# Optimization experiments

Hardware: AMD Instinct MI355X
Metric: run time of the kernel (lower is better)

Reference implementation:

```python
import math
import jax, jax.numpy as jnp
import numpy as np

N = 50000
C = 128      # in_channels == out_channels
H = 8        # nhead
D = C // H   # head_dim = 16
E = 800000


def _layernorm(x, g, b, eps=1e-5):
    mu = jnp.mean(x, axis=-1, keepdims=True)
    var = jnp.var(x, axis=-1, keepdims=True)
    return (x - mu) * jax.lax.rsqrt(var + eps) * g + b


def setup_inputs() -> dict:
    key = jax.random.key(0)
    ks = jax.random.split(key, 12)
    s = 1.0 / math.sqrt(C)          # ~xavier scale
    s4 = 1.0 / math.sqrt(4 * C)
    return {
        "x": jax.random.normal(ks[0], (N, C), dtype=jnp.float32),
        "edge_index": jax.random.randint(ks[1], (2, E), 0, N, dtype=jnp.int64),
        "Wq": jax.random.normal(ks[2], (C, C), dtype=jnp.float32) * s,
        "Wk": jax.random.normal(ks[3], (C, C), dtype=jnp.float32) * s,
        "Wv": jax.random.normal(ks[4], (C, C), dtype=jnp.float32) * s,
        "Wo": jax.random.normal(ks[5], (C, C), dtype=jnp.float32) * s,
        "bo": jnp.zeros((C,), dtype=jnp.float32),
        "Wf1": jax.random.normal(ks[6], (C, 4 * C), dtype=jnp.float32) * s,
        "bf1": jnp.zeros((4 * C,), dtype=jnp.float32),
        "Wf2": jax.random.normal(ks[7], (4 * C, C), dtype=jnp.float32) * s4,
        "bf2": jnp.zeros((C,), dtype=jnp.float32),
        "g1": jnp.ones((C,), dtype=jnp.float32),
        "b1": jnp.zeros((C,), dtype=jnp.float32),
        "g2": jnp.ones((C,), dtype=jnp.float32),
        "b2": jnp.zeros((C,), dtype=jnp.float32),
    }


def reference(x, edge_index, Wq, Wk, Wv, Wo, bo, Wf1, bf1, Wf2, bf2, g1, b1, g2, b2):
    n = x.shape[0]
    loops = jnp.arange(n, dtype=edge_index.dtype)
    row = jnp.concatenate([edge_index[0], loops])  # source nodes
    col = jnp.concatenate([edge_index[1], loops])  # destination nodes

    q = (x @ Wq).reshape(n, H, D)
    k = (x @ Wk).reshape(n, H, D)
    v = (x @ Wv).reshape(n, H, D)

    # edge-level attention scores [E+N, H]
    scores = jnp.einsum('ehd,ehd->eh', q[row], k[col]) / math.sqrt(D)
    smax = jax.ops.segment_max(scores, col, num_segments=n)  # every node has a self-loop
    exp = jnp.exp(scores - smax[col])
    ssum = jax.ops.segment_sum(exp, col, num_segments=n)
    alpha = exp / (ssum[col] + 1e-8)

    out = jax.ops.segment_sum(v[row] * alpha[..., None], col, num_segments=n)
    attn = out.reshape(n, C) @ Wo + bo

    residual = x  # input_proj is Identity (in_channels == out_channels)
    x1 = _layernorm(residual + attn, g1, b1)
    ffn = jax.nn.gelu(x1 @ Wf1 + bf1, approximate=False) @ Wf2 + bf2
    return _layernorm(x1 + ffn, g2, b2)
```

## Files before the change

kernel.cpp:

```cpp
#include <hip/hip_runtime.h>
#include <cmath>


typedef short bf16x8 __attribute__((ext_vector_type(8)));
typedef float f32x4 __attribute__((ext_vector_type(4)));
typedef unsigned int uint_as1 __attribute__((address_space(1)));
typedef unsigned int uint_as3 __attribute__((address_space(3)));

__device__ inline unsigned short f2bf(float f) {
    unsigned int u = __float_as_uint(f);
    u += 0x7fffu + ((u >> 16) & 1u);
    return (unsigned short)(u >> 16);
}
__device__ inline float bflo(unsigned int w) { return __uint_as_float(w << 16); }
__device__ inline float bfhi(unsigned int w) { return __uint_as_float(w & 0xffff0000u); }

__device__ inline void gload16(const unsigned short* g, unsigned short* l) {
    __builtin_amdgcn_global_load_lds((const uint_as1*)g, (uint_as3*)l, 16, 0, 0);
}

__device__ inline float gelu_f(float x) {
    float ax = fabsf(x) * 0.70710678118f;
    float t = __builtin_amdgcn_rcpf(fmaf(0.3275911f, ax, 1.0f));
    float p = fmaf(1.061405429f, t, -1.453152027f);
    p = fmaf(p, t, 1.421413741f);
    p = fmaf(p, t, -0.284496736f);
    p = fmaf(p, t, 0.254829592f);
    p = p * t;
    float e = __expf(-ax * ax);
    float pe = p * e;
    float w = (x >= 0.f) ? (2.0f - pe) : pe;
    return 0.5f * x * w;
}


__device__ __forceinline__ void stage_panel(unsigned short* Bs,
                                            const unsigned short* base,
                                            int strideK) {
    int tid = threadIdx.x;
    int srow = tid >> 4, cc = tid & 15;
    int gc = (cc & ~7) | ((cc & 7) ^ (srow & 7));
    const unsigned short* src = base + (size_t)srow * strideK + gc * 8;
    unsigned short* dst = Bs + srow * 128 + cc * 8;
#pragma unroll
    for (int j = 0; j < 8; ++j)
        gload16(src + (size_t)j * 16 * strideK, dst + j * 16 * 128);
}

__device__ __forceinline__ void loadA_g(bf16x8 (&af)[4][4],
                                        const unsigned short* A, int M,
                                        int m0, int wr, int l16, int quad) {
#pragma unroll
    for (int ti = 0; ti < 4; ++ti) {
        int row = m0 + wr * 64 + ti * 16 + l16;
        if (row > M - 1) row = M - 1;
        const unsigned short* ar = A + (size_t)row * 128 + quad * 8;
#pragma unroll
        for (int j = 0; j < 4; ++j) af[ti][j] = *(const bf16x8*)(ar + j * 32);
    }
}

__device__ __forceinline__ void mm16(f32x4 (&acc)[4][4], const bf16x8 (&af)[4][4],
                                     const unsigned short* Bs,
                                     int wc, int quad, int l16) {
#pragma unroll
    for (int ks = 0; ks < 4; ++ks) {
        bf16x8 bfr[4];
#pragma unroll
        for (int tj = 0; tj < 4; ++tj) {
            int nr = wc * 64 + tj * 16 + l16;
            int cidx = ks * 4 + quad;
            int slot = (cidx & ~7) | ((cidx & 7) ^ (nr & 7));
            bfr[tj] = *(const bf16x8*)&Bs[nr * 128 + slot * 8];
        }
#pragma unroll
        for (int ti = 0; ti < 4; ++ti)
#pragma unroll
            for (int tj = 0; tj < 4; ++tj)
                acc[ti][tj] = __builtin_amdgcn_mfma_f32_16x16x32_bf16(
                    af[ti][ks], bfr[tj], acc[ti][tj], 0, 0, 0);
    }
}


__global__ __launch_bounds__(256) void k_init(
    const float* __restrict__ x, unsigned short* __restrict__ xb,
    const float* __restrict__ Wq, const float* __restrict__ Wk,
    const float* __restrict__ Wv, const float* __restrict__ Wo,
    const float* __restrict__ Wf1, const float* __restrict__ Wf2,
    unsigned short* __restrict__ Wqkvt, unsigned short* __restrict__ Wot,
    unsigned short* __restrict__ Wf1t, unsigned short* __restrict__ Wf2t,
    int* __restrict__ cursor, int4* __restrict__ csrz,
    int N, int nCsr4, int nCast) {
    int bid = blockIdx.x;
    int t = threadIdx.x;

    int NBc = (N + 255) >> 8;
    if (bid < NBc) {
        int i = bid * 256 + t;
        if (i < N) cursor[i] = 0;
        return;
    }
    bid -= NBc;
    int NBz = (nCsr4 + 255) >> 8;
    if (bid < NBz) {
        int i = bid * 256 + t;
        if (i < nCsr4) csrz[i] = make_int4(0, 0, 0, 0);
        return;
    }
    bid -= NBz;
    if (bid < nCast) {
        int i = bid * 256 + t;
        if (i < N * 32) {
            float4 v = ((const float4*)x)[i];
            ushort4 o;
            o.x = f2bf(v.x); o.y = f2bf(v.y); o.z = f2bf(v.z); o.w = f2bf(v.w);
            ((ushort4*)xb)[i] = o;
        }
        return;
    }
    bid -= nCast;
    int z, idx;
    if (bid < 256) { z = bid >> 6; idx = (bid & 63) * 256 + t; }
    else           { z = 4 + ((bid - 256) >> 8); idx = ((bid - 256) & 255) * 256 + t; }

    const float* in; unsigned short* out; int K, Co;
    switch (z) {
        case 0: in = Wq;  out = Wqkvt; K = 128; Co = 128; break;
        case 1: in = Wk;  out = Wqkvt; K = 128; Co = 128; break;
        case 2: in = Wv;  out = Wqkvt; K = 128; Co = 128; break;
        case 3: in = Wo;  out = Wot;   K = 128; Co = 128; break;
        case 4: in = Wf1; out = Wf1t;  K = 128; Co = 512; break;
        default: in = Wf2; out = Wf2t; K = 512; Co = 128; break;
    }
    if (idx >= K * Co) return;
    int k = idx / Co, c = idx % Co;
    int row;
    switch (z) {
        case 0: row = ((c >> 1) << 2) | (c & 1); break;
        case 1: row = 256 + c; break;
        case 2: row = (((c >> 1) << 2) | (c & 1)) + 2; break;
        default: row = c; break;
    }
    out[(size_t)row * K + k] = f2bf(in[idx]);
}


__global__ __launch_bounds__(256) void k_fq(
    const int* __restrict__ ei, int* __restrict__ cursor,
    unsigned short* __restrict__ csr, int E, int N,
    const unsigned short* __restrict__ xb, const unsigned short* __restrict__ Wqkvt,
    unsigned short* __restrict__ qkv, int nFillB, int Mt) {
    __shared__ unsigned short smem[128 * 136];

    if ((int)blockIdx.x < nFillB) {
        int e = blockIdx.x * 256 + threadIdx.x;
        if (e < E + N) {
            int row, col;
            if (e < E) { row = ei[e]; col = ei[E + e]; }
            else       { row = col = e - E; }
            int pos = atomicAdd(&cursor[col], 1);
            csr[(size_t)col * 64 + pos] = (unsigned short)row;
        }
        return;
    }

    int bid = blockIdx.x - nFillB;
    int z = bid / Mt, mt = bid % Mt;
    int m0 = mt * 128, n0 = z * 128;

    int tid = threadIdx.x;
    int wid = tid >> 6, lane = tid & 63;
    int quad = lane >> 4, l16 = lane & 15;
    int wr = wid >> 1, wc = wid & 1;

    bf16x8 af[4][4];
    loadA_g(af, xb, N, m0, wr, l16, quad);
    stage_panel(smem, Wqkvt + (size_t)n0 * 128, 128);
    __syncthreads();

    f32x4 acc[4][4];
#pragma unroll
    for (int i = 0; i < 4; ++i)
#pragma unroll
        for (int j = 0; j < 4; ++j) acc[i][j] = {0.f, 0.f, 0.f, 0.f};
    mm16(acc, af, smem, wc, quad, l16);

    __syncthreads();
#pragma unroll
    for (int ti = 0; ti < 4; ++ti)
#pragma unroll
        for (int tj = 0; tj < 4; ++tj) {
            int c = wc * 64 + tj * 16 + l16;
#pragma unroll
            for (int r = 0; r < 4; ++r) {
                int rl = wr * 64 + ti * 16 + quad * 4 + r;
                smem[rl * 136 + c] = f2bf(acc[ti][tj][r]);
            }
        }
    __syncthreads();
    int rl = tid >> 1, half = tid & 1;
    int grow = m0 + rl;
    if (grow < N) {
#pragma unroll
        for (int c8 = 0; c8 < 8; ++c8) {
            uint4 v = *(const uint4*)&smem[rl * 136 + half * 64 + c8 * 8];
            *(uint4*)&qkv[(size_t)grow * 384 + n0 + half * 64 + c8 * 8] = v;
        }
    }
}


__global__ __launch_bounds__(256) void k_attn(
    const unsigned int* __restrict__ qkv, const int* __restrict__ counts,
    const unsigned short* __restrict__ csr, unsigned int* __restrict__ ob,
    int N) {
    int j = blockIdx.x * 4 + (threadIdx.x >> 6);
    if (j >= N) return;
    int l = threadIdx.x & 63;
    int lk = l & 31;
    int half = l >> 5;
    const uint4* qv4 = (const uint4*)qkv;

    uint2 kw = *(const uint2*)(qkv + (size_t)j * 192 + 128 + lk * 2);
    const float S = 0.36067376022224085f;
    float k0 = bflo(kw.x) * S, k1 = bfhi(kw.x) * S;
    float k2 = bflo(kw.y) * S, k3 = bfhi(kw.y) * S;

    int cnt = counts[j];
    int nb = (cnt + 3) >> 2;
    const unsigned short* cp = csr + (size_t)j * 64;

    int ra0 = cp[half],     rb0 = cp[2 + half];
    int ra1 = cp[4 + half], rb1 = cp[6 + half];
    uint4 gA = qv4[(unsigned)ra0 * 48u + lk];
    uint4 gB = qv4[(unsigned)rb0 * 48u + lk];

    float lsum = 0.f, a0 = 0.f, a1 = 0.f, a2 = 0.f, a3 = 0.f;
    for (int bi = 0; bi < nb; ++bi) {
        int ra2 = cp[(bi + 2) * 4 + half];
        int rb2 = cp[(bi + 2) * 4 + 2 + half];
        uint4 nA = qv4[(unsigned)ra1 * 48u + lk];
        uint4 nB = qv4[(unsigned)rb1 * 48u + lk];

        int rem = cnt - bi * 4;
        {
            float s = fmaf(bflo(gA.x), k0,
                      fmaf(bfhi(gA.x), k1,
                      fmaf(bflo(gA.z), k2, bfhi(gA.z) * k3)));
            s += __shfl_xor(s, 1);
            s += __shfl_xor(s, 2);
            float e = exp2f(s);
            e = (half < rem) ? e : 0.f;
            lsum += e;
            a0 = fmaf(e, bflo(gA.y), a0); a1 = fmaf(e, bfhi(gA.y), a1);
            a2 = fmaf(e, bflo(gA.w), a2); a3 = fmaf(e, bfhi(gA.w), a3);
        }
        {
            float s = fmaf(bflo(gB.x), k0,
                      fmaf(bfhi(gB.x), k1,
                      fmaf(bflo(gB.z), k2, bfhi(gB.z) * k3)));
            s += __shfl_xor(s, 1);
            s += __shfl_xor(s, 2);
            float e = exp2f(s);
            e = (2 + half < rem) ? e : 0.f;
            lsum += e;
            a0 = fmaf(e, bflo(gB.y), a0); a1 = fmaf(e, bfhi(gB.y), a1);
            a2 = fmaf(e, bflo(gB.w), a2); a3 = fmaf(e, bfhi(gB.w), a3);
        }
        gA = nA; gB = nB; ra1 = ra2; rb1 = rb2;
    }

    lsum += __shfl_xor(lsum, 32);
    a0 += __shfl_xor(a0, 32); a1 += __shfl_xor(a1, 32);
    a2 += __shfl_xor(a2, 32); a3 += __shfl_xor(a3, 32);

    if (half == 0) {
        float inv = 1.f / (lsum + 1e-8f);
        uint2 o;
        o.x = ((unsigned int)f2bf(a1 * inv) << 16) | (unsigned int)f2bf(a0 * inv);
        o.y = ((unsigned int)f2bf(a3 * inv) << 16) | (unsigned int)f2bf(a2 * inv);
        *(uint2*)(ob + (size_t)j * 64 + lk * 2) = o;
    }
}


__global__ __launch_bounds__(256) void k_tail(
    const unsigned short* __restrict__ ob, const unsigned short* __restrict__ Wot,
    const float* __restrict__ bo, const float* __restrict__ x,
    const float* __restrict__ g1, const float* __restrict__ b1,
    const unsigned short* __restrict__ Wf1t, const float* __restrict__ bf1,
    const unsigned short* __restrict__ Wf2t, const float* __restrict__ bf2,
    const float* __restrict__ g2, const float* __restrict__ b2,
    float* __restrict__ dout, int M) {
    __shared__ unsigned short Bs[128 * 128];
    __shared__ unsigned short Ls[128 * 136];
    __shared__ float X1[128 * 132];
    __shared__ float pS[2][128], pQ[2][128];

    int tid = threadIdx.x;
    int wid = tid >> 6, lane = tid & 63;
    int quad = lane >> 4, l16 = lane & 15;
    int wr = wid >> 1, wc = wid & 1;
    int m0 = blockIdx.x * 128;

    float gv1[4], bv1[4], gv2[4], bv2[4], bi[4];
#pragma unroll
    for (int tj = 0; tj < 4; ++tj) {
        int col = wc * 64 + tj * 16 + l16;
        gv1[tj] = g1[col]; bv1[tj] = b1[col];
        gv2[tj] = g2[col]; bv2[tj] = b2[col];
        bi[tj] = bo[col];
    }

    {
        bf16x8 af[4][4];
        loadA_g(af, ob, M, m0, wr, l16, quad);
        stage_panel(Bs, Wot, 128);
        __syncthreads();

        f32x4 acc[4][4];
#pragma unroll
        for (int i = 0; i < 4; ++i)
#pragma unroll
            for (int j = 0; j < 4; ++j) acc[i][j] = {0.f, 0.f, 0.f, 0.f};
        mm16(acc, af, Bs, wc, quad, l16);

#pragma unroll
        for (int ti = 0; ti < 4; ++ti)
#pragma unroll
            for (int tj = 0; tj < 4; ++tj) {
                int col = wc * 64 + tj * 16 + l16;
#pragma unroll
                for (int r = 0; r < 4; ++r) {
                    int row = m0 + wr * 64 + ti * 16 + quad * 4 + r;
                    float rv = (row < M) ? x[(size_t)row * 128 + col] : 0.f;
                    acc[ti][tj][r] += bi[tj] + rv;
                }
            }
#pragma unroll
        for (int ti = 0; ti < 4; ++ti)
#pragma unroll
            for (int r = 0; r < 4; ++r) {
                float s = acc[ti][0][r] + acc[ti][1][r] + acc[ti][2][r] + acc[ti][3][r];
                float q = acc[ti][0][r] * acc[ti][0][r] + acc[ti][1][r] * acc[ti][1][r]
                        + acc[ti][2][r] * acc[ti][2][r] + acc[ti][3][r] * acc[ti][3][r];
                s += __shfl_xor(s, 1); q += __shfl_xor(q, 1);
                s += __shfl_xor(s, 2); q += __shfl_xor(q, 2);
                s += __shfl_xor(s, 4); q += __shfl_xor(q, 4);
                s += __shfl_xor(s, 8); q += __shfl_xor(q, 8);
                if (l16 == 0) {
                    int lr = wr * 64 + ti * 16 + quad * 4 + r;
                    pS[wc][lr] = s; pQ[wc][lr] = q;
                }
            }
        __syncthreads();
        if (tid < 128) {
            float s = pS[0][tid] + pS[1][tid];
            float q = pQ[0][tid] + pQ[1][tid];
            float mean = s * 0.0078125f;
            float var = q * 0.0078125f - mean * mean;
            pS[0][tid] = mean;
            pQ[0][tid] = rsqrtf(var + 1e-5f);
        }
        __syncthreads();
#pragma unroll
        for (int ti = 0; ti < 4; ++ti)
#pragma unroll
            for (int r = 0; r < 4; ++r) {
                int lr = wr * 64 + ti * 16 + quad * 4 + r;
                float mean = pS[0][lr], rs = pQ[0][lr];
#pragma unroll
                for (int tj = 0; tj < 4; ++tj) {
                    int col = wc * 64 + tj * 16 + l16;
                    float y = (acc[ti][tj][r] - mean) * rs * gv1[tj] + bv1[tj];
                    X1[lr * 132 + col] = y;
                    Ls[lr * 136 + col] = f2bf(y);
                }
            }
    }
    __syncthreads();

    bf16x8 ax1[4][4];
#pragma unroll
    for (int ti = 0; ti < 4; ++ti) {
        int rl = wr * 64 + ti * 16 + l16;
#pragma unroll
        for (int j = 0; j < 4; ++j)
            ax1[ti][j] = *(const bf16x8*)&Ls[rl * 136 + j * 32 + quad * 8];
    }

    f32x4 dacc[4][4];
#pragma unroll
    for (int i = 0; i < 4; ++i)
#pragma unroll
        for (int j = 0; j < 4; ++j) dacc[i][j] = {0.f, 0.f, 0.f, 0.f};

    for (int c = 0; c < 4; ++c) {
        __syncthreads();
        stage_panel(Bs, Wf1t + (size_t)c * 128 * 128, 128);
        __syncthreads();

        f32x4 hacc[4][4];
#pragma unroll
        for (int i = 0; i < 4; ++i)
#pragma unroll
            for (int j = 0; j < 4; ++j) hacc[i][j] = {0.f, 0.f, 0.f, 0.f};
        mm16(hacc, ax1, Bs, wc, quad, l16);

#pragma unroll
        for (int ti = 0; ti < 4; ++ti)
#pragma unroll
            for (int tj = 0; tj < 4; ++tj) {
                float bb = bf1[c * 128 + wc * 64 + tj * 16 + l16];
#pragma unroll
                for (int r = 0; r < 4; ++r) {
                    int rl = wr * 64 + ti * 16 + quad * 4 + r;
                    Ls[rl * 136 + wc * 64 + tj * 16 + l16] =
                        f2bf(gelu_f(hacc[ti][tj][r] + bb));
                }
            }
        __syncthreads();

        bf16x8 ah[4][4];
#pragma unroll
        for (int ti = 0; ti < 4; ++ti) {
            int rl = wr * 64 + ti * 16 + l16;
#pragma unroll
            for (int j = 0; j < 4; ++j)
                ah[ti][j] = *(const bf16x8*)&Ls[rl * 136 + j * 32 + quad * 8];
        }
        __syncthreads();
        stage_panel(Bs, Wf2t + (size_t)c * 128, 512);
        __syncthreads();
        mm16(dacc, ah, Bs, wc, quad, l16);
    }

#pragma unroll
    for (int ti = 0; ti < 4; ++ti)
#pragma unroll
        for (int tj = 0; tj < 4; ++tj) {
            int col = wc * 64 + tj * 16 + l16;
            float bb = bf2[col];
#pragma unroll
            for (int r = 0; r < 4; ++r) {
                int lr = wr * 64 + ti * 16 + quad * 4 + r;
                dacc[ti][tj][r] += bb + X1[lr * 132 + col];
            }
        }
#pragma unroll
    for (int ti = 0; ti < 4; ++ti)
#pragma unroll
        for (int r = 0; r < 4; ++r) {
            float s = dacc[ti][0][r] + dacc[ti][1][r] + dacc[ti][2][r] + dacc[ti][3][r];
            float q = dacc[ti][0][r] * dacc[ti][0][r] + dacc[ti][1][r] * dacc[ti][1][r]
                    + dacc[ti][2][r] * dacc[ti][2][r] + dacc[ti][3][r] * dacc[ti][3][r];
            s += __shfl_xor(s, 1); q += __shfl_xor(q, 1);
            s += __shfl_xor(s, 2); q += __shfl_xor(q, 2);
            s += __shfl_xor(s, 4); q += __shfl_xor(q, 4);
            s += __shfl_xor(s, 8); q += __shfl_xor(q, 8);
            if (l16 == 0) {
                int lr = wr * 64 + ti * 16 + quad * 4 + r;
                pS[wc][lr] = s; pQ[wc][lr] = q;
            }
        }
    __syncthreads();
    if (tid < 128) {
        float s = pS[0][tid] + pS[1][tid];
        float q = pQ[0][tid] + pQ[1][tid];
        float mean = s * 0.0078125f;
        float var = q * 0.0078125f - mean * mean;
        pS[0][tid] = mean;
        pQ[0][tid] = rsqrtf(var + 1e-5f);
    }
    __syncthreads();
#pragma unroll
    for (int ti = 0; ti < 4; ++ti)
#pragma unroll
        for (int r = 0; r < 4; ++r) {
            int lr = wr * 64 + ti * 16 + quad * 4 + r;
            int row = m0 + lr;
            if (row >= M) continue;
            float mean = pS[0][lr], rs = pQ[0][lr];
#pragma unroll
            for (int tj = 0; tj < 4; ++tj) {
                int col = wc * 64 + tj * 16 + l16;
                dout[(size_t)row * 128 + col] =
                    (dacc[ti][tj][r] - mean) * rs * gv2[tj] + bv2[tj];
            }
        }
}


extern "C" void kernel_launch(void* const* d_in, const int* in_sizes, int n_in,
                              void* d_out, int out_size, void* d_ws, size_t ws_size,
                              hipStream_t stream) {
    const float* x   = (const float*)d_in[0];
    const int* ei    = (const int*)d_in[1];
    const float* Wq  = (const float*)d_in[2];
    const float* Wk  = (const float*)d_in[3];
    const float* Wv  = (const float*)d_in[4];
    const float* Wo  = (const float*)d_in[5];
    const float* bo  = (const float*)d_in[6];
    const float* Wf1 = (const float*)d_in[7];
    const float* bf1 = (const float*)d_in[8];
    const float* Wf2 = (const float*)d_in[9];
    const float* bf2 = (const float*)d_in[10];
    const float* g1  = (const float*)d_in[11];
    const float* b1  = (const float*)d_in[12];
    const float* g2  = (const float*)d_in[13];
    const float* b2  = (const float*)d_in[14];

    int N = in_sizes[0] / 128;
    int E = in_sizes[1] / 2;
    int N2 = ((N + 127) / 128) * 128;
    int NE = E + N;

    char* p = (char*)d_ws;
    auto alloc = [&](size_t bytes) -> char* {
        char* r = p;
        p += (bytes + 255) & ~(size_t)255;
        return r;
    };
    unsigned short* qkv = (unsigned short*)alloc((size_t)N2 * 384 * 2);
    unsigned short* ob  = (unsigned short*)alloc((size_t)N2 * 128 * 2);
    unsigned short* xb  = (unsigned short*)alloc((size_t)N2 * 128 * 2);
    unsigned short* Wqkvt = (unsigned short*)alloc(384 * 128 * 2);
    unsigned short* Wot   = (unsigned short*)alloc(128 * 128 * 2);
    unsigned short* Wf1t  = (unsigned short*)alloc(512 * 128 * 2);
    unsigned short* Wf2t  = (unsigned short*)alloc(128 * 512 * 2);
    int* cursor = (int*)alloc((size_t)N * 4);
    unsigned short* csr = (unsigned short*)alloc(((size_t)N * 64 + 256) * 2);

    int nCsr4 = N * 8 + 32;
    int nCast = (N * 32 + 255) / 256;
    int nInit = ((N + 255) / 256) + ((nCsr4 + 255) / 256) + nCast + 768;
    int M128 = (N + 127) / 128;
    int nFillB = (NE + 255) / 256;

    k_init<<<nInit, 256, 0, stream>>>(x, xb, Wq, Wk, Wv, Wo, Wf1, Wf2,
                                      Wqkvt, Wot, Wf1t, Wf2t,
                                      cursor, (int4*)csr, N, nCsr4, nCast);

    k_fq<<<nFillB + 3 * M128, 256, 0, stream>>>(ei, cursor, csr, E, N,
                                                xb, Wqkvt, qkv, nFillB, M128);

    k_attn<<<(N + 3) / 4, 256, 0, stream>>>((const unsigned int*)qkv, cursor,
                                            csr, (unsigned int*)ob, N);

    k_tail<<<M128, 256, 0, stream>>>(ob, Wot, bo, x, g1, b1,
                                     Wf1t, bf1, Wf2t, bf2, g2, b2,
                                     (float*)d_out, N);
}
```

Baseline: 349.2 us.

## Cut k_tail LDS footprint for two blocks per CU and interleave CSR fill with QKV GEMM

k_tail drops its padded Ls and fp32 X1 shared buffers. The LayerNorm-1 output is written to a new global fp32 buffer and read back for the second residual. The GELU hidden tile is kept in a swizzled LDS buffer and consumed by a new mm16_AL that loads A fragments straight from LDS. With the smaller LDS use and launch_bounds(256,2), two blocks can share a CU. Separately, k_fq interleaves edge-fill blocks with GEMM blocks (one GEMM per four block ids) so atomics and matmul overlap, at the cost of extra global traffic for x1 and some redundant empty blocks.

```diff
diff --git a/kernel.cpp b/kernel.cpp
--- a/kernel.cpp
+++ b/kernel.cpp
@@ -82,6 +82,36 @@
     }
 }
 
+__device__ __forceinline__ void mm16_AL(f32x4 (&acc)[4][4],
+                                        const unsigned short* Hs,
+                                        const unsigned short* Bs,
+                                        int wr, int wc, int quad, int l16) {
+#pragma unroll
+    for (int ks = 0; ks < 4; ++ks) {
+        int cidx = ks * 4 + quad;
+        bf16x8 afr[4];
+#pragma unroll
+        for (int ti = 0; ti < 4; ++ti) {
+            int rl = wr * 64 + ti * 16 + l16;
+            int slot = (cidx & ~7) | ((cidx & 7) ^ (rl & 7));
+            afr[ti] = *(const bf16x8*)&Hs[rl * 128 + slot * 8];
+        }
+        bf16x8 bfr[4];
+#pragma unroll
+        for (int tj = 0; tj < 4; ++tj) {
+            int nr = wc * 64 + tj * 16 + l16;
+            int slot = (cidx & ~7) | ((cidx & 7) ^ (nr & 7));
+            bfr[tj] = *(const bf16x8*)&Bs[nr * 128 + slot * 8];
+        }
+#pragma unroll
+        for (int ti = 0; ti < 4; ++ti)
+#pragma unroll
+            for (int tj = 0; tj < 4; ++tj)
+                acc[ti][tj] = __builtin_amdgcn_mfma_f32_16x16x32_bf16(
+                    afr[ti], bfr[tj], acc[ti][tj], 0, 0, 0);
+    }
+}
+
 
 __global__ __launch_bounds__(256) void k_init(
     const float* __restrict__ x, unsigned short* __restrict__ xb,
@@ -153,8 +183,11 @@
     unsigned short* __restrict__ qkv, int nFillB, int Mt) {
     __shared__ unsigned short smem[128 * 136];
 
-    if ((int)blockIdx.x < nFillB) {
-        int e = blockIdx.x * 256 + threadIdx.x;
+    int bid = blockIdx.x;
+    if (bid & 3) {
+        int fi = bid - (bid >> 2) - 1;
+        if (fi >= nFillB) return;
+        int e = fi * 256 + threadIdx.x;
         if (e < E + N) {
             int row, col;
             if (e < E) { row = ei[e]; col = ei[E + e]; }
@@ -165,8 +198,8 @@
         return;
     }
 
-    int bid = blockIdx.x - nFillB;
-    int z = bid / Mt, mt = bid % Mt;
+    int qb = bid >> 2;
+    int z = qb / Mt, mt = qb % Mt;
     int m0 = mt * 128, n0 = z * 128;
 
     int tid = threadIdx.x;
@@ -285,17 +318,17 @@
 }
 
 
-__global__ __launch_bounds__(256) void k_tail(
+__global__ __launch_bounds__(256, 2) void k_tail(
     const unsigned short* __restrict__ ob, const unsigned short* __restrict__ Wot,
     const float* __restrict__ bo, const float* __restrict__ x,
     const float* __restrict__ g1, const float* __restrict__ b1,
+    float* __restrict__ x1f,
     const unsigned short* __restrict__ Wf1t, const float* __restrict__ bf1,
     const unsigned short* __restrict__ Wf2t, const float* __restrict__ bf2,
     const float* __restrict__ g2, const float* __restrict__ b2,
     float* __restrict__ dout, int M) {
     __shared__ unsigned short Bs[128 * 128];
-    __shared__ unsigned short Ls[128 * 136];
-    __shared__ float X1[128 * 132];
+    __shared__ unsigned short Hs[128 * 128];
     __shared__ float pS[2][128], pQ[2][128];
 
     int tid = threadIdx.x;
@@ -304,15 +337,6 @@
     int wr = wid >> 1, wc = wid & 1;
     int m0 = blockIdx.x * 128;
 
-    float gv1[4], bv1[4], gv2[4], bv2[4], bi[4];
-#pragma unroll
-    for (int tj = 0; tj < 4; ++tj) {
-        int col = wc * 64 + tj * 16 + l16;
-        gv1[tj] = g1[col]; bv1[tj] = b1[col];
-        gv2[tj] = g2[col]; bv2[tj] = b2[col];
-        bi[tj] = bo[col];
-    }
-
     {
         bf16x8 af[4][4];
         loadA_g(af, ob, M, m0, wr, l16, quad);
@@ -331,11 +355,12 @@
 #pragma unroll
             for (int tj = 0; tj < 4; ++tj) {
                 int col = wc * 64 + tj * 16 + l16;
+                float bb = bo[col];
 #pragma unroll
                 for (int r = 0; r < 4; ++r) {
                     int row = m0 + wr * 64 + ti * 16 + quad * 4 + r;
                     float rv = (row < M) ? x[(size_t)row * 128 + col] : 0.f;
-                    acc[ti][tj][r] += bi[tj] + rv;
+                    acc[ti][tj][r] += bb + rv;
                 }
             }
 #pragma unroll
@@ -369,13 +394,16 @@
 #pragma unroll
             for (int r = 0; r < 4; ++r) {
                 int lr = wr * 64 + ti * 16 + quad * 4 + r;
+                int row = m0 + lr;
                 float mean = pS[0][lr], rs = pQ[0][lr];
 #pragma unroll
                 for (int tj = 0; tj < 4; ++tj) {
                     int col = wc * 64 + tj * 16 + l16;
-                    float y = (acc[ti][tj][r] - mean) * rs * gv1[tj] + bv1[tj];
-                    X1[lr * 132 + col] = y;
-                    Ls[lr * 136 + col] = f2bf(y);
+                    float y = (acc[ti][tj][r] - mean) * rs * g1[col] + b1[col];
+                    if (row < M) x1f[(size_t)row * 128 + col] = y;
+                    int ch = col >> 3;
+                    int sc = (ch & ~7) | ((ch & 7) ^ (lr & 7));
+                    Hs[lr * 128 + sc * 8 + (col & 7)] = f2bf(y);
                 }
             }
     }
@@ -386,8 +414,11 @@
     for (int ti = 0; ti < 4; ++ti) {
         int rl = wr * 64 + ti * 16 + l16;
 #pragma unroll
-        for (int j = 0; j < 4; ++j)
-            ax1[ti][j] = *(const bf16x8*)&Ls[rl * 136 + j * 32 + quad * 8];
+        for (int j = 0; j < 4; ++j) {
+            int cidx = j * 4 + quad;
+            int slot = (cidx & ~7) | ((cidx & 7) ^ (rl & 7));
+            ax1[ti][j] = *(const bf16x8*)&Hs[rl * 128 + slot * 8];
+        }
     }
 
     f32x4 dacc[4][4];
@@ -407,33 +438,27 @@
 #pragma unroll
             for (int j = 0; j < 4; ++j) hacc[i][j] = {0.f, 0.f, 0.f, 0.f};
         mm16(hacc, ax1, Bs, wc, quad, l16);
+        __syncthreads();
 
 #pragma unroll
         for (int ti = 0; ti < 4; ++ti)
 #pragma unroll
             for (int tj = 0; tj < 4; ++tj) {
-                float bb = bf1[c * 128 + wc * 64 + tj * 16 + l16];
+                int cc = wc * 64 + tj * 16 + l16;
+                float bb = bf1[c * 128 + cc];
 #pragma unroll
                 for (int r = 0; r < 4; ++r) {
                     int rl = wr * 64 + ti * 16 + quad * 4 + r;
-                    Ls[rl * 136 + wc * 64 + tj * 16 + l16] =
+                    int ch = cc >> 3;
+                    int sc = (ch & ~7) | ((ch & 7) ^ (rl & 7));
+                    Hs[rl * 128 + sc * 8 + (cc & 7)] =
                         f2bf(gelu_f(hacc[ti][tj][r] + bb));
                 }
             }
-        __syncthreads();
-
-        bf16x8 ah[4][4];
-#pragma unroll
-        for (int ti = 0; ti < 4; ++ti) {
-            int rl = wr * 64 + ti * 16 + l16;
-#pragma unroll
-            for (int j = 0; j < 4; ++j)
-                ah[ti][j] = *(const bf16x8*)&Ls[rl * 136 + j * 32 + quad * 8];
-        }
-        __syncthreads();
         stage_panel(Bs, Wf2t + (size_t)c * 128, 512);
         __syncthreads();
-        mm16(dacc, ah, Bs, wc, quad, l16);
+
+        mm16_AL(dacc, Hs, Bs, wr, wc, quad, l16);
     }
 
 #pragma unroll
@@ -444,8 +469,9 @@
             float bb = bf2[col];
 #pragma unroll
             for (int r = 0; r < 4; ++r) {
-                int lr = wr * 64 + ti * 16 + quad * 4 + r;
-                dacc[ti][tj][r] += bb + X1[lr * 132 + col];
+                int row = m0 + wr * 64 + ti * 16 + quad * 4 + r;
+                float rv = (row < M) ? x1f[(size_t)row * 128 + col] : 0.f;
+                dacc[ti][tj][r] += bb + rv;
             }
         }
 #pragma unroll
@@ -486,7 +512,7 @@
             for (int tj = 0; tj < 4; ++tj) {
                 int col = wc * 64 + tj * 16 + l16;
                 dout[(size_t)row * 128 + col] =
-                    (dacc[ti][tj][r] - mean) * rs * gv2[tj] + bv2[tj];
+                    (dacc[ti][tj][r] - mean) * rs * g2[col] + b2[col];
             }
         }
 }
@@ -525,6 +551,7 @@
     unsigned short* qkv = (unsigned short*)alloc((size_t)N2 * 384 * 2);
     unsigned short* ob  = (unsigned short*)alloc((size_t)N2 * 128 * 2);
     unsigned short* xb  = (unsigned short*)alloc((size_t)N2 * 128 * 2);
+    float* x1f          = (float*)alloc((size_t)N2 * 128 * 4);
     unsigned short* Wqkvt = (unsigned short*)alloc(384 * 128 * 2);
     unsigned short* Wot   = (unsigned short*)alloc(128 * 128 * 2);
     unsigned short* Wf1t  = (unsigned short*)alloc(512 * 128 * 2);
@@ -537,18 +564,19 @@
     int nInit = ((N + 255) / 256) + ((nCsr4 + 255) / 256) + nCast + 768;
     int M128 = (N + 127) / 128;
     int nFillB = (NE + 255) / 256;
+    int nQkv = 3 * M128;
 
     k_init<<<nInit, 256, 0, stream>>>(x, xb, Wq, Wk, Wv, Wo, Wf1, Wf2,
                                       Wqkvt, Wot, Wf1t, Wf2t,
                                       cursor, (int4*)csr, N, nCsr4, nCast);
 
-    k_fq<<<nFillB + 3 * M128, 256, 0, stream>>>(ei, cursor, csr, E, N,
-                                                xb, Wqkvt, qkv, nFillB, M128);
+    k_fq<<<4 * nQkv, 256, 0, stream>>>(ei, cursor, csr, E, N,
+                                       xb, Wqkvt, qkv, nFillB, M128);
 
     k_attn<<<(N + 3) / 4, 256, 0, stream>>>((const unsigned int*)qkv, cursor,
                                             csr, (unsigned int*)ob, N);
 
-    k_tail<<<M128, 256, 0, stream>>>(ob, Wot, bo, x, g1, b1,
+    k_tail<<<M128, 256, 0, stream>>>(ob, Wot, bo, x, g1, b1, x1f,
                                      Wf1t, bf1, Wf2t, bf2, g2, b2,
                                      (float*)d_out, N);
 }
```

Result: slower. 424.8 us (+21.6%).
